# Optimization experiments

Measured on AMD Instinct MI355X. Metric: run time of the kernel, lower is better.

## Reference

```python
import math
import jax, jax.numpy as jnp
import numpy as np

DIM = 512; DEPTH = 12; HEADS = 8; DIM_HEAD = 64
INNER = HEADS * DIM_HEAD
FF_INNER = 4 * DIM
B = 8192
NUM_TIMESTEPS = 1000
SCALE = 16.0  # cosine_sim_scale
ROT_DIM = 32  # RotaryEmbedding(dim=min(32, dim_head))
NUM_BUCKETS = 32; MAX_DISTANCE = 128


def layer_norm(x, g, eps=1e-5):
    mean = jnp.mean(x, axis=-1, keepdims=True)
    var = jnp.mean((x - mean) ** 2, axis=-1, keepdims=True)  # unbiased=False
    return (x - mean) * jax.lax.rsqrt(var + eps) * g


def l2norm(t):
    n = jnp.linalg.norm(t, axis=-1, keepdims=True)
    return t / jnp.maximum(n, 1e-12)


def rotary_freqs(n):
    inv = 1.0 / (10000.0 ** (jnp.arange(0, ROT_DIM, 2, dtype=jnp.float32) / ROT_DIM))
    f = jnp.arange(n, dtype=jnp.float32)[:, None] * inv[None, :]  # (n, ROT_DIM//2)
    return jnp.repeat(f, 2, axis=-1)  # (n, ROT_DIM), interleaved pairs


def rotate_half(x):
    x1 = x[..., 0::2]; x2 = x[..., 1::2]
    return jnp.stack((-x2, x1), axis=-1).reshape(x.shape)


def apply_rotary(t, freqs):
    tr, tp = t[..., :ROT_DIM], t[..., ROT_DIM:]
    tr = tr * jnp.cos(freqs) + rotate_half(tr) * jnp.sin(freqs)
    return jnp.concatenate([tr, tp], axis=-1)


def rel_pos_bias(i, j, emb):
    rel = jnp.arange(j)[None, :] - jnp.arange(i)[:, None]
    n = jnp.maximum(-rel, 0)
    max_exact = NUM_BUCKETS // 2
    nf = jnp.maximum(n, 1).astype(jnp.float32)
    val_large = max_exact + (jnp.log(nf / max_exact) / math.log(MAX_DISTANCE / max_exact) * (NUM_BUCKETS - max_exact)).astype(jnp.int32)
    val_large = jnp.minimum(val_large, NUM_BUCKETS - 1)
    bucket = jnp.where(n < max_exact, n, val_large)
    return emb[bucket].transpose(2, 0, 1)  # (h, i, j)


def setup_inputs() -> dict:
    key = jax.random.key(0)
    ks = jax.random.split(key, 13)
    w = 0.02
    return {
        "image_embed": jax.random.normal(ks[0], (B, DIM), jnp.float32),
        "text_embed": jax.random.normal(ks[1], (B, DIM), jnp.float32),
        "timesteps": jax.random.randint(ks[2], (B,), 0, NUM_TIMESTEPS),
        "time_emb_table": jax.random.normal(ks[3], (NUM_TIMESTEPS, DIM)) * w,
        "learned_query": jax.random.normal(ks[4], (DIM,)),
        "rel_emb": jax.random.normal(ks[5], (NUM_BUCKETS, HEADS)) * w,
        "attn_norm_g": jnp.ones((DEPTH, DIM)),
        "Wq": jax.random.normal(ks[6], (DEPTH, DIM, INNER)) * w,
        "Wkv": jax.random.normal(ks[7], (DEPTH, DIM, 2 * DIM_HEAD)) * w,
        "null_kv": jax.random.normal(ks[8], (DEPTH, 2, DIM_HEAD)),
        "Wo": jax.random.normal(ks[9], (DEPTH, INNER, DIM)) * w,
        "attn_out_norm_g": jnp.ones((DEPTH, DIM)),
        "ff_norm_g": jnp.ones((DEPTH, DIM)),
        "Wff1": jax.random.normal(ks[10], (DEPTH, DIM, 2 * FF_INNER)) * w,
        "Wff2": jax.random.normal(ks[11], (DEPTH, FF_INNER, DIM)) * w,
        "final_norm_g": jnp.ones((DIM,)),
        "Wproj": jax.random.normal(ks[12], (DIM, DIM)) * w,
    }


def reference(image_embed, text_embed, timesteps, time_emb_table, learned_query, rel_emb,
              attn_norm_g, Wq, Wkv, null_kv, Wo, attn_out_norm_g,
              ff_norm_g, Wff1, Wff2, final_norm_g, Wproj):
    b = image_embed.shape[0]
    # token sequence: [text_embed, time_embed, image_embed, learned_query] -> (b, 4, dim)
    tokens = jnp.concatenate([
        text_embed[:, None, :],
        time_emb_table[timesteps][:, None, :],
        image_embed[:, None, :],
        jnp.broadcast_to(learned_query, (b, 1, DIM)),
    ], axis=1)
    n = tokens.shape[1]
    bias = rel_pos_bias(n, n + 1, rel_emb)            # (h, n, n+1)
    freqs = rotary_freqs(n)                           # (n, ROT_DIM)
    causal = jnp.triu(jnp.ones((n, n + 1), dtype=bool), k=2)
    neg = -jnp.finfo(jnp.float32).max
    sqrt_scale = math.sqrt(SCALE)

    x = tokens
    for l in range(DEPTH):
        # --- Attention ---
        h = layer_norm(x, attn_norm_g[l])
        q = (h @ Wq[l]).reshape(b, n, HEADS, DIM_HEAD).transpose(0, 2, 1, 3) * SCALE
        kv = h @ Wkv[l]
        k, v = kv[..., :DIM_HEAD], kv[..., DIM_HEAD:]  # single-head kv (b, n, d)
        q = apply_rotary(q, freqs)
        k = apply_rotary(k, freqs)
        nk = jnp.broadcast_to(null_kv[l, 0], (b, 1, DIM_HEAD))
        nv = jnp.broadcast_to(null_kv[l, 1], (b, 1, DIM_HEAD))
        k = jnp.concatenate([nk, k], axis=1)
        v = jnp.concatenate([nv, v], axis=1)
        q = l2norm(q) * sqrt_scale
        k = l2norm(k) * sqrt_scale
        sim = jnp.einsum('bhid,bjd->bhij', q, k) + bias[None]
        sim = jnp.where(causal[None, None], neg, sim)
        attn = jax.nn.softmax(sim.astype(jnp.float32), axis=-1).astype(sim.dtype)
        out = jnp.einsum('bhij,bjd->bhid', attn, v).transpose(0, 2, 1, 3).reshape(b, n, INNER)
        x = x + layer_norm(out @ Wo[l], attn_out_norm_g[l])
        # --- SwiGLU FFN ---
        h = layer_norm(x, ff_norm_g[l])
        hg = h @ Wff1[l]
        a, g = hg[..., :FF_INNER], hg[..., FF_INNER:]
        x = x + (a * jax.nn.silu(g)) @ Wff2[l]

    x = layer_norm(x, final_norm_g) @ Wproj
    return x[:, -1, :]  # predicted image embed from learned query position
```

## Files before the change

kernel.cpp:

```cpp
#include <hip/hip_runtime.h>

typedef __bf16 bf16x8 __attribute__((ext_vector_type(8)));
typedef __bf16 bf16x4 __attribute__((ext_vector_type(4)));
typedef __bf16 bf16x2 __attribute__((ext_vector_type(2)));
typedef float  f32x4  __attribute__((ext_vector_type(4)));
typedef unsigned short u16;

#define BATCH   8192
#define NTOK    4
#define ROWS    (BATCH*NTOK)
#define DIM     512
#define HEADS   8
#define DH      64
#define FFI     2048
#define DEPTH   12
#define LN_EPS  1e-5f

static const size_t OFF_WQKV = 0;
static const size_t SZ_WQKV  = 12ull*640*512*2;
static const size_t OFF_WTO  = OFF_WQKV + SZ_WQKV;
static const size_t SZ_WTO   = 12ull*512*512*2;
static const size_t OFF_WTF1 = OFF_WTO + SZ_WTO;
static const size_t SZ_WTF1  = 12ull*4096*512*2;
static const size_t OFF_WTF2 = OFF_WTF1 + SZ_WTF1;
static const size_t SZ_WTF2  = 12ull*512*2048*2;
static const size_t OFF_WTP  = OFF_WTF2 + SZ_WTF2;
static const size_t SZ_WTP   = 512ull*512*2;
static const size_t OFF_X    = OFF_WTP + SZ_WTP;
static const size_t OFF_H    = OFF_X    + (size_t)ROWS*DIM*4;
static const size_t OFF_QKV  = OFF_H    + (size_t)ROWS*DIM*2;
static const size_t OFF_AO   = OFF_QKV  + (size_t)ROWS*640*2;
static const size_t OFF_FLAG = OFF_AO   + (size_t)ROWS*DIM*2;
static const size_t WS_NEED  = OFF_FLAG + 256;

__device__ __forceinline__ float ldf(const void* p, size_t i, bool b16) {
  return b16 ? (float)((const __bf16*)p)[i] : ((const float*)p)[i];
}

__device__ __forceinline__ void gld_lds16(const void* g, void* l) {
  __builtin_amdgcn_global_load_lds((const __attribute__((address_space(1))) void*)g,
                                   (__attribute__((address_space(3))) void*)l, 16, 0, 0);
}

__device__ __forceinline__ float gsum16(float v) {
  #pragma unroll
  for (int o = 8; o > 0; o >>= 1) v += __shfl_xor(v, o, 64);
  return v;
}

__device__ __forceinline__ void block_reduce2(float& a, float& b, float* sm) {
  #pragma unroll
  for (int o = 32; o > 0; o >>= 1) { a += __shfl_down(a, o, 64); b += __shfl_down(b, o, 64); }
  int lane = threadIdx.x & 63, w = threadIdx.x >> 6;
  __syncthreads();
  if (lane == 0) { sm[w] = a; sm[4+w] = b; }
  __syncthreads();
  a = sm[0]+sm[1]+sm[2]+sm[3];
  b = sm[4]+sm[5]+sm[6]+sm[7];
}

__global__ void detect_dtype(const unsigned int* __restrict__ w, int* __restrict__ flag) {
  __shared__ int cnt[4];
  int t = threadIdx.x;
  int c = 0;
  for (int i = t; i < 2048; i += 256) {
    unsigned int v = w[i];
    unsigned int lo = v & 0xFFFFu, hi = v >> 16;
    int elo = (int)((lo >> 7) & 0xFF), ehi = (int)((hi >> 7) & 0xFF);
    bool okl = (lo == 0u) || (elo >= 100 && elo <= 140);
    bool okh = (hi == 0u) || (ehi >= 100 && ehi <= 140);
    if (okl && okh) c++;
  }
  #pragma unroll
  for (int o = 32; o > 0; o >>= 1) c += __shfl_down(c, o, 64);
  if ((t & 63) == 0) cnt[t >> 6] = c;
  __syncthreads();
  if (t == 0) flag[0] = (cnt[0] + cnt[1] + cnt[2] + cnt[3] > 1024) ? 1 : 0;
}

__global__ void transpose_any(const void* __restrict__ in, u16* __restrict__ out,
                              int K, int N, size_t out_zsz, int rowoff, int mode,
                              const int* __restrict__ flag) {
  bool b16 = flag[0] != 0;
  __shared__ u16 tile[32][33];
  size_t iboff = (size_t)blockIdx.z * K * N;
  size_t oboff = (size_t)blockIdx.z * out_zsz;
  int n0 = blockIdx.x * 32, k0 = blockIdx.y * 32;
  int tx = threadIdx.x, ty = threadIdx.y;
  #pragma unroll
  for (int r = 0; r < 4; r++) {
    float v = ldf(in, iboff + (size_t)(k0 + ty*4 + r) * N + n0 + tx, b16);
    __bf16 bv = (__bf16)v;
    tile[ty*4+r][tx] = __builtin_bit_cast(u16, bv);
  }
  __syncthreads();
  int rbase;
  if (mode == 0) rbase = rowoff + n0;
  else {
    int s = (n0 >= 2048) ? 1 : 0;
    int np = n0 - s*2048;
    rbase = (np >> 7)*256 + ((np >> 5) & 3)*64 + s*32;
  }
  #pragma unroll
  for (int r = 0; r < 4; r++)
    out[oboff + (size_t)(rbase + ty*4 + r) * K + k0 + tx] = tile[tx][ty*4+r];
}

__global__ void build_tokens(const void* __restrict__ text, const void* __restrict__ img,
                             const int* __restrict__ ts, const void* __restrict__ table,
                             const void* __restrict__ lq, float* __restrict__ x,
                             const int* __restrict__ flag) {
  bool b16 = flag[0] != 0;
  int b = blockIdx.x, t = threadIdx.x;
  float* xr = x + (size_t)b * NTOK * DIM;
  int tsb = ts[b];
  for (int e = t; e < DIM; e += 256) {
    xr[e]         = ldf(text,  (size_t)b * DIM + e, b16);
    xr[DIM + e]   = ldf(table, (size_t)tsb * DIM + e, b16);
    xr[2*DIM + e] = ldf(img,   (size_t)b * DIM + e, b16);
    xr[3*DIM + e] = ldf(lq,    (size_t)e, b16);
  }
}

__global__ void ln_f32_bf16(const float* __restrict__ x, const void* __restrict__ g, size_t goff,
                            __bf16* __restrict__ out, const int* __restrict__ flag) {
  bool b16 = flag[0] != 0;
  __shared__ float sm[8];
  int row = blockIdx.x, t = threadIdx.x;
  float2 v = ((const float2*)(x + (size_t)row * DIM))[t];
  float s = v.x + v.y, s2 = v.x*v.x + v.y*v.y;
  block_reduce2(s, s2, sm);
  float mean = s * (1.f/DIM);
  float var  = s2 * (1.f/DIM) - mean*mean;
  float rs = rsqrtf(var + LN_EPS);
  float g0 = ldf(g, goff + 2*t, b16), g1 = ldf(g, goff + 2*t + 1, b16);
  bf16x2 o2 = { (__bf16)((v.x-mean)*rs*g0), (__bf16)((v.y-mean)*rs*g1) };
  ((bf16x2*)(out + (size_t)row * DIM))[t] = o2;
}

__global__ void ln_add_ln(const __bf16* __restrict__ y,
                          const void* __restrict__ g1, size_t g1off,
                          const void* __restrict__ g2, size_t g2off,
                          float* __restrict__ x, __bf16* __restrict__ h,
                          const int* __restrict__ flag) {
  bool b16 = flag[0] != 0;
  __shared__ float sm[8];
  int row = blockIdx.x, t = threadIdx.x;
  bf16x2 yv = ((const bf16x2*)(y + (size_t)row * DIM))[t];
  float v0 = (float)yv[0], v1 = (float)yv[1];
  float s = v0 + v1, s2 = v0*v0 + v1*v1;
  block_reduce2(s, s2, sm);
  float mean = s * (1.f/DIM);
  float var  = s2 * (1.f/DIM) - mean*mean;
  float rs = rsqrtf(var + LN_EPS);
  float ga = ldf(g1, g1off + 2*t, b16), gb = ldf(g1, g1off + 2*t + 1, b16);
  float2* xr = (float2*)(x + (size_t)row * DIM);
  float2 xv = xr[t];
  xv.x += (v0-mean)*rs*ga;
  xv.y += (v1-mean)*rs*gb;
  xr[t] = xv;
  float s_  = xv.x + xv.y, s2_ = xv.x*xv.x + xv.y*xv.y;
  block_reduce2(s_, s2_, sm);
  float mean2 = s_ * (1.f/DIM);
  float var2  = s2_ * (1.f/DIM) - mean2*mean2;
  float rs2 = rsqrtf(var2 + LN_EPS);
  float gc = ldf(g2, g2off + 2*t, b16), gd = ldf(g2, g2off + 2*t + 1, b16);
  bf16x2 o2 = { (__bf16)((xv.x-mean2)*rs2*gc), (__bf16)((xv.y-mean2)*rs2*gd) };
  ((bf16x2*)(h + (size_t)row * DIM))[t] = o2;
}

__global__ void ln_final(const float* __restrict__ x, const void* __restrict__ g,
                         __bf16* __restrict__ out, const int* __restrict__ flag) {
  bool b16 = flag[0] != 0;
  __shared__ float sm[8];
  int b = blockIdx.x, t = threadIdx.x;
  int row = b*NTOK + 3;
  float2 v = ((const float2*)(x + (size_t)row * DIM))[t];
  float s = v.x + v.y, s2 = v.x*v.x + v.y*v.y;
  block_reduce2(s, s2, sm);
  float mean = s * (1.f/DIM);
  float var  = s2 * (1.f/DIM) - mean*mean;
  float rs = rsqrtf(var + LN_EPS);
  float g0 = ldf(g, (size_t)2*t, b16), g1 = ldf(g, (size_t)2*t + 1, b16);
  bf16x2 o2 = { (__bf16)((v.x-mean)*rs*g0), (__bf16)((v.y-mean)*rs*g1) };
  ((bf16x2*)(out + (size_t)b * DIM))[t] = o2;
}

template<int BROWS, int EPI>
__global__ __launch_bounds__(512, 2) void gemm8(
    const __bf16* __restrict__ A, int lda,
    const __bf16* __restrict__ B, int ldb,
    void* __restrict__ Cv, int ldc, int K, const int* __restrict__ flag)
{
  constexpr int UNITS = (BROWS == 256) ? 4 : 3;
  constexpr int WCN   = (BROWS == 256) ? 4 : 2;
  constexpr int M_FR  = (BROWS == 256) ? 8 : 4;
  constexpr int QM    = M_FR / 4;
  __shared__ char ldsmem[2][(256 + BROWS) * 128];

  const int tid = threadIdx.x;
  const int wid = tid >> 6, lane = tid & 63;
  const int wr = wid / WCN, wc = wid % WCN;
  const int lr = lane & 15, lc = lane >> 4;
  const int sr = tid >> 3;
  const int cs = ((tid & 7) ^ (sr & 7)) * 8;
  const int bx = blockIdx.x, by = blockIdx.y;

  const __bf16* Ab = A + (size_t)by * 256 * lda;
  const __bf16* Bb = B + (size_t)bx * BROWS * ldb;

  f32x4 acc[M_FR][4] = {};
  const int NT = K >> 6;

  char* lds0 = ldsmem[0];
  char* lds1 = ldsmem[1];

  auto stage_unit = [&](int p, int kt, int u) {
    char* base = (p ? lds1 : lds0);
    if (u < 2) {
      const __bf16* s = Ab + (size_t)(u*128 + sr) * lda + kt*64 + cs;
      char* d = base + u*16384 + (wid << 10);
      gld_lds16(s, d);
      gld_lds16(s + (size_t)64 * lda, d + 8192);
    } else {
      const __bf16* s = Bb + (size_t)((u-2)*128 + sr) * ldb + kt*64 + cs;
      char* d = base + 32768 + (u-2)*16384 + (wid << 10);
      gld_lds16(s, d);
      gld_lds16(s + (size_t)64 * ldb, d + 8192);
    }
  };

  #pragma unroll
  for (int u = 0; u < UNITS; u++) stage_unit(0, 0, u);

  const int NIT = NT >> 1;
  for (int i = 0; i < NIT; i++) {
    const int t1 = 2*i + 1;
    const int t2 = (2*i + 2 < NT) ? (2*i + 2) : 0;
    #pragma unroll
    for (int hfl = 0; hfl < 2; hfl++) {
      char* cbase = hfl ? lds1 : lds0;
      const int sp = hfl ^ 1;
      const int st = hfl ? t2 : t1;
      bf16x8 bfr[4][2];
      #pragma unroll
      for (int q = 0; q < 4; q++) {
        if (q < UNITS) stage_unit(sp, st, q);
        if (q == 0) {
          asm volatile("s_waitcnt vmcnt(2)" ::: "memory");
          asm volatile("s_barrier" ::: "memory");
          #pragma unroll
          for (int f = 0; f < 4; f++)
            #pragma unroll
            for (int kk = 0; kk < 2; kk++) {
              int row = wc*64 + f*16 + lr;
              int ch = (kk*4 + lc) ^ (lr & 7);
              bfr[f][kk] = *(const bf16x8*)(cbase + 32768 + row*128 + ch*16);
            }
        }
        bf16x8 afr[QM][2];
        #pragma unroll
        for (int m2 = 0; m2 < QM; m2++)
          #pragma unroll
          for (int kk = 0; kk < 2; kk++) {
            int row = wr*(M_FR*16) + (q*QM + m2)*16 + lr;
            int ch = (kk*4 + lc) ^ (lr & 7);
            afr[m2][kk] = *(const bf16x8*)(cbase + row*128 + ch*16);
          }
        __builtin_amdgcn_s_setprio(1);
        #pragma unroll
        for (int m2 = 0; m2 < QM; m2++)
          #pragma unroll
          for (int n = 0; n < 4; n++)
            #pragma unroll
            for (int kk = 0; kk < 2; kk++)
              acc[q*QM + m2][n] = __builtin_amdgcn_mfma_f32_16x16x32_bf16(
                  afr[m2][kk], bfr[n][kk], acc[q*QM + m2][n], 0, 0, 0);
        __builtin_amdgcn_s_setprio(0);
        asm volatile("s_barrier" ::: "memory");
      }
    }
  }

  if (EPI == 1) {
    __bf16* Ob = (__bf16*)Cv;
    const int colb = bx*128 + wc*32 + lr;
    const int rowb = by*256 + wr*128 + lc*4;
    #pragma unroll
    for (int m = 0; m < M_FR; m++)
      #pragma unroll
      for (int rr = 0; rr < 4; rr++) {
        size_t ro = (size_t)(rowb + m*16 + rr) * ldc;
        #pragma unroll
        for (int fa = 0; fa < 2; fa++) {
          float a = acc[m][fa][rr], g = acc[m][fa+2][rr];
          Ob[ro + colb + fa*16] = (__bf16)(a * g / (1.f + __expf(-g)));
        }
      }
  } else if (EPI == 2) {
    float* Xf = (float*)Cv;
    const int colb = bx*BROWS + wc*64 + lr;
    const int rowb = by*256 + wr*(M_FR*16) + lc*4;
    #pragma unroll
    for (int m = 0; m < M_FR; m++)
      #pragma unroll
      for (int rr = 0; rr < 4; rr++) {
        size_t ro = (size_t)(rowb + m*16 + rr) * ldc;
        #pragma unroll
        for (int n = 0; n < 4; n++) Xf[ro + colb + n*16] += acc[m][n][rr];
      }
  } else if (EPI == 0) {
    __bf16* Cb = (__bf16*)Cv;
    const int colb = bx*BROWS + wc*64 + lr;
    const int rowb = by*256 + wr*(M_FR*16) + lc*4;
    #pragma unroll
    for (int m = 0; m < M_FR; m++)
      #pragma unroll
      for (int rr = 0; rr < 4; rr++) {
        size_t ro = (size_t)(rowb + m*16 + rr) * ldc;
        #pragma unroll
        for (int n = 0; n < 4; n++) Cb[ro + colb + n*16] = (__bf16)acc[m][n][rr];
      }
  } else {
    bool b16o = flag[0] != 0;
    __bf16* Cb = (__bf16*)Cv;
    float*  Cf = (float*)Cv;
    const int colb = bx*BROWS + wc*64 + lr;
    const int rowb = by*256 + wr*(M_FR*16) + lc*4;
    #pragma unroll
    for (int m = 0; m < M_FR; m++)
      #pragma unroll
      for (int rr = 0; rr < 4; rr++) {
        size_t ro = (size_t)(rowb + m*16 + rr) * ldc;
        #pragma unroll
        for (int n = 0; n < 4; n++) {
          float val = acc[m][n][rr];
          if (b16o) Cb[ro + colb + n*16] = (__bf16)val; else Cf[ro + colb + n*16] = val;
        }
      }
  }
}

__global__ __launch_bounds__(256) void attn_kernel(
    const __bf16* __restrict__ qkv,
    const void* __restrict__ nkv_all, int layer, const void* __restrict__ rel_emb,
    __bf16* __restrict__ ao, const int* __restrict__ flag)
{
  bool b16 = flag[0] != 0;
  const int tid = threadIdx.x;
  const int w = tid >> 6, l = tid & 63;
  const int g = l >> 4, c = l & 15;
  const int bh = blockIdx.x * 16 + w * 4 + g;
  const int b = bh >> 3, h = bh & 7;
  const bool rot = (c < 8);

  const float LN1E4_32 = 9.210340371976184f * (1.f/32.f);
  float inv0 = __expf(-(float)(4*c)     * LN1E4_32);
  float inv1 = __expf(-(float)(4*c + 2) * LN1E4_32);
  float cs0[4], sn0[4], cs1[4], sn1[4];
  #pragma unroll
  for (int t = 0; t < 4; t++) {
    __sincosf((float)t * inv0, &sn0[t], &cs0[t]);
    __sincosf((float)t * inv1, &sn1[t], &cs1[t]);
  }
  float rb[4];
  #pragma unroll
  for (int t = 0; t < 4; t++) rb[t] = ldf(rel_emb, (size_t)t * 8 + h, b16);

  float q[4][4];
  #pragma unroll
  for (int i = 0; i < 4; i++) {
    bf16x4 qv = *(const bf16x4*)(qkv + ((size_t)(b*NTOK + i)) * 640 + h*DH + c*4);
    float v0 = (float)qv[0], v1 = (float)qv[1], v2 = (float)qv[2], v3 = (float)qv[3];
    if (rot) {
      float n0 = v0*cs0[i] - v1*sn0[i], n1 = v1*cs0[i] + v0*sn0[i];
      float n2 = v2*cs1[i] - v3*sn1[i], n3 = v3*cs1[i] + v2*sn1[i];
      v0 = n0; v1 = n1; v2 = n2; v3 = n3;
    }
    q[i][0] = v0; q[i][1] = v1; q[i][2] = v2; q[i][3] = v3;
  }
  #pragma unroll
  for (int i = 0; i < 4; i++) {
    float ss = q[i][0]*q[i][0] + q[i][1]*q[i][1] + q[i][2]*q[i][2] + q[i][3]*q[i][3];
    float r = 1.f / fmaxf(sqrtf(gsum16(ss)), 1e-12f);
    #pragma unroll
    for (int e = 0; e < 4; e++) q[i][e] *= r;
  }

  float kk[5][4], vv[5][4];
  #pragma unroll
  for (int e = 0; e < 4; e++) {
    kk[0][e] = ldf(nkv_all, (size_t)layer*128 + c*4 + e, b16);
    vv[0][e] = ldf(nkv_all, (size_t)layer*128 + 64 + c*4 + e, b16);
  }
  #pragma unroll
  for (int j = 1; j < 5; j++) {
    const __bf16* base = qkv + ((size_t)(b*NTOK + j - 1)) * 640 + 512;
    bf16x4 kv4 = *(const bf16x4*)(base + c*4);
    bf16x4 vv4 = *(const bf16x4*)(base + 64 + c*4);
    float v0 = (float)kv4[0], v1 = (float)kv4[1], v2 = (float)kv4[2], v3 = (float)kv4[3];
    if (rot) {
      int t = j - 1;
      float n0 = v0*cs0[t] - v1*sn0[t], n1 = v1*cs0[t] + v0*sn0[t];
      float n2 = v2*cs1[t] - v3*sn1[t], n3 = v3*cs1[t] + v2*sn1[t];
      v0 = n0; v1 = n1; v2 = n2; v3 = n3;
    }
    kk[j][0] = v0; kk[j][1] = v1; kk[j][2] = v2; kk[j][3] = v3;
    #pragma unroll
    for (int e = 0; e < 4; e++) vv[j][e] = (float)vv4[e];
  }
  #pragma unroll
  for (int j = 0; j < 5; j++) {
    float ss = kk[j][0]*kk[j][0] + kk[j][1]*kk[j][1] + kk[j][2]*kk[j][2] + kk[j][3]*kk[j][3];
    float r = 1.f / fmaxf(sqrtf(gsum16(ss)), 1e-12f);
    #pragma unroll
    for (int e = 0; e < 4; e++) kk[j][e] *= r;
  }

  #pragma unroll
  for (int i = 0; i < 4; i++) {
    float sim[5];
    #pragma unroll
    for (int j = 0; j < 5; j++) {
      if (j > i + 1) break;
      float pp = q[i][0]*kk[j][0] + q[i][1]*kk[j][1] + q[i][2]*kk[j][2] + q[i][3]*kk[j][3];
      sim[j] = 16.f * gsum16(pp) + rb[(i - j > 0) ? (i - j) : 0];
    }
    float m = sim[0];
    #pragma unroll
    for (int j = 1; j < 5; j++) { if (j > i + 1) break; m = fmaxf(m, sim[j]); }
    float Z = 0.f, o0 = 0.f, o1 = 0.f, o2 = 0.f, o3 = 0.f;
    #pragma unroll
    for (int j = 0; j < 5; j++) {
      if (j > i + 1) break;
      float e = __expf(sim[j] - m);
      Z += e;
      o0 += e * vv[j][0]; o1 += e * vv[j][1]; o2 += e * vv[j][2]; o3 += e * vv[j][3];
    }
    float rz = 1.f / Z;
    bf16x4 ov = { (__bf16)(o0*rz), (__bf16)(o1*rz), (__bf16)(o2*rz), (__bf16)(o3*rz) };
    *(bf16x4*)(ao + ((size_t)(b*NTOK + i)) * DIM + h*DH + c*4) = ov;
  }
}

extern "C" void kernel_launch(void* const* d_in, const int* in_sizes, int n_in,
                              void* d_out, int out_size, void* d_ws, size_t ws_size,
                              hipStream_t stream) {
  const void* image_embed     = d_in[0];
  const void* text_embed      = d_in[1];
  const int*  timesteps       = (const int*)d_in[2];
  const void* time_table      = d_in[3];
  const void* learned_query   = d_in[4];
  const void* rel_emb         = d_in[5];
  const void* attn_norm_g     = d_in[6];
  const void* Wq              = d_in[7];
  const void* Wkv             = d_in[8];
  const void* null_kv         = d_in[9];
  const void* Wo              = d_in[10];
  const void* attn_out_norm_g = d_in[11];
  const void* ff_norm_g       = d_in[12];
  const void* Wff1            = d_in[13];
  const void* Wff2            = d_in[14];
  const void* final_norm_g    = d_in[15];
  const void* Wproj           = d_in[16];

  if (ws_size < WS_NEED) return;

  char* ws = (char*)d_ws;
  __bf16* wqkv = (__bf16*)(ws + OFF_WQKV);
  __bf16* wto  = (__bf16*)(ws + OFF_WTO);
  __bf16* wtf1 = (__bf16*)(ws + OFF_WTF1);
  __bf16* wtf2 = (__bf16*)(ws + OFF_WTF2);
  __bf16* wtp  = (__bf16*)(ws + OFF_WTP);
  float*  x    = (float*) (ws + OFF_X);
  __bf16* h    = (__bf16*)(ws + OFF_H);
  __bf16* qkv  = (__bf16*)(ws + OFF_QKV);
  __bf16* ao   = (__bf16*)(ws + OFF_AO);
  __bf16* act  = (__bf16*)(ws + OFF_QKV);
  int*    flag = (int*)   (ws + OFF_FLAG);

  detect_dtype<<<1, 256, 0, stream>>>((const unsigned int*)Wq, flag);

  dim3 tb(32, 8);
  transpose_any<<<dim3(16, 16, 12),  tb, 0, stream>>>(Wq,   (u16*)wqkv, 512,  512,  640ull*512, 0,   0, flag);
  transpose_any<<<dim3(4,  16, 12),  tb, 0, stream>>>(Wkv,  (u16*)wqkv, 512,  128,  640ull*512, 512, 0, flag);
  transpose_any<<<dim3(16, 16, 12),  tb, 0, stream>>>(Wo,   (u16*)wto,  512,  512,  512ull*512, 0,   0, flag);
  transpose_any<<<dim3(128,16, 12),  tb, 0, stream>>>(Wff1, (u16*)wtf1, 512,  4096, 4096ull*512,0,   1, flag);
  transpose_any<<<dim3(16, 64, 12),  tb, 0, stream>>>(Wff2, (u16*)wtf2, 2048, 512,  512ull*2048,0,   0, flag);
  transpose_any<<<dim3(16, 16, 1),   tb, 0, stream>>>(Wproj,(u16*)wtp,  512,  512,  512ull*512, 0,   0, flag);

  build_tokens<<<BATCH, 256, 0, stream>>>(text_embed, image_embed, timesteps, time_table,
                                          learned_query, x, flag);

  for (int l = 0; l < DEPTH; l++) {
    const __bf16* wqkv_l = wqkv + (size_t)l * 640 * 512;
    const __bf16* wto_l  = wto  + (size_t)l * 512 * 512;
    const __bf16* wtf1_l = wtf1 + (size_t)l * 4096 * 512;
    const __bf16* wtf2_l = wtf2 + (size_t)l * 512 * 2048;

    ln_f32_bf16<<<ROWS, 256, 0, stream>>>(x, attn_norm_g, (size_t)l*DIM, h, flag);
    gemm8<128,0><<<dim3(5, 128), 512, 0, stream>>>(h, DIM, wqkv_l, 512, qkv, 640, 512, flag);
    attn_kernel<<<BATCH/2, 256, 0, stream>>>(qkv, null_kv, l, rel_emb, ao, flag);
    gemm8<128,0><<<dim3(4, 128), 512, 0, stream>>>(ao, DIM, wto_l, 512, qkv , DIM, 512, flag);
    ln_add_ln<<<ROWS, 256, 0, stream>>>(qkv , attn_out_norm_g, (size_t)l*DIM,
                                        ff_norm_g, (size_t)l*DIM, x, h, flag);

    for (int c = 0; c < 2; c++) {
      const __bf16* hc = h + (size_t)c * 16384 * DIM;
      float*        xc = x + (size_t)c * 16384 * DIM;
      gemm8<256,1><<<dim3(16, 64), 512, 0, stream>>>(hc, DIM, wtf1_l, 512, act, FFI, 512, flag);
      gemm8<128,2><<<dim3(4, 64), 512, 0, stream>>>(act, FFI, wtf2_l, FFI, xc, DIM, 2048, flag);
    }
  }

  ln_final<<<BATCH, 256, 0, stream>>>(x, final_norm_g, ao , flag);
  gemm8<128,3><<<dim3(4, 32), 512, 0, stream>>>(ao, DIM, wtp, 512, d_out, DIM, 512, flag);
}
```

Baseline: 5.390 ms.

## Use one wavefront per row for layernorms and simplify GEMM K-loop pipeline

The layernorm kernels now assign one 64-lane wavefront per row with 8 elements per lane. Reductions use only wave shuffles, with vectorized float4 and bf16x8 loads and stores in place of block-level LDS reductions and two barriers, so the grid shrinks by 4x. The GEMM main loop is rewritten from an interleaved staged-per-quarter pipeline to a simpler per-k-tile double buffer: it issues all loads for the next tile up front, then waits and computes. This may lose the finer-grained overlap of loads with MFMA work that the old schedule had.

After: 5.809 ms. +7.8%, slower.

```diff
diff --git a/kernel.cpp b/kernel.cpp
--- a/kernel.cpp
+++ b/kernel.cpp
@@ -48,15 +48,9 @@
   return v;
 }
 
-__device__ __forceinline__ void block_reduce2(float& a, float& b, float* sm) {
-  #pragma unroll
-  for (int o = 32; o > 0; o >>= 1) { a += __shfl_down(a, o, 64); b += __shfl_down(b, o, 64); }
-  int lane = threadIdx.x & 63, w = threadIdx.x >> 6;
-  __syncthreads();
-  if (lane == 0) { sm[w] = a; sm[4+w] = b; }
-  __syncthreads();
-  a = sm[0]+sm[1]+sm[2]+sm[3];
-  b = sm[4]+sm[5]+sm[6]+sm[7];
+__device__ __forceinline__ void wred2(float& a, float& b) {
+  #pragma unroll
+  for (int o = 32; o > 0; o >>= 1) { a += __shfl_xor(a, o, 64); b += __shfl_xor(b, o, 64); }
 }
 
 __global__ void detect_dtype(const unsigned int* __restrict__ w, int* __restrict__ flag) {
@@ -125,17 +119,23 @@
 __global__ void ln_f32_bf16(const float* __restrict__ x, const void* __restrict__ g, size_t goff,
                             __bf16* __restrict__ out, const int* __restrict__ flag) {
   bool b16 = flag[0] != 0;
-  __shared__ float sm[8];
-  int row = blockIdx.x, t = threadIdx.x;
-  float2 v = ((const float2*)(x + (size_t)row * DIM))[t];
-  float s = v.x + v.y, s2 = v.x*v.x + v.y*v.y;
-  block_reduce2(s, s2, sm);
+  int lane = threadIdx.x & 63;
+  int row = blockIdx.x * 4 + (threadIdx.x >> 6);
+  const float4* xr = (const float4*)(x + (size_t)row * DIM);
+  float4 A4 = xr[lane*2], B4 = xr[lane*2 + 1];
+  float v[8] = {A4.x, A4.y, A4.z, A4.w, B4.x, B4.y, B4.z, B4.w};
+  float s = 0.f, s2 = 0.f;
+  #pragma unroll
+  for (int e = 0; e < 8; e++) { s += v[e]; s2 += v[e]*v[e]; }
+  wred2(s, s2);
   float mean = s * (1.f/DIM);
   float var  = s2 * (1.f/DIM) - mean*mean;
   float rs = rsqrtf(var + LN_EPS);
-  float g0 = ldf(g, goff + 2*t, b16), g1 = ldf(g, goff + 2*t + 1, b16);
-  bf16x2 o2 = { (__bf16)((v.x-mean)*rs*g0), (__bf16)((v.y-mean)*rs*g1) };
-  ((bf16x2*)(out + (size_t)row * DIM))[t] = o2;
+  bf16x8 ov;
+  #pragma unroll
+  for (int e = 0; e < 8; e++)
+    ov[e] = (__bf16)((v[e]-mean) * rs * ldf(g, goff + lane*8 + e, b16));
+  *(bf16x8*)(out + (size_t)row * DIM + lane*8) = ov;
 }
 
 __global__ void ln_add_ln(const __bf16* __restrict__ y,
@@ -144,46 +144,60 @@
                           float* __restrict__ x, __bf16* __restrict__ h,
                           const int* __restrict__ flag) {
   bool b16 = flag[0] != 0;
-  __shared__ float sm[8];
-  int row = blockIdx.x, t = threadIdx.x;
-  bf16x2 yv = ((const bf16x2*)(y + (size_t)row * DIM))[t];
-  float v0 = (float)yv[0], v1 = (float)yv[1];
-  float s = v0 + v1, s2 = v0*v0 + v1*v1;
-  block_reduce2(s, s2, sm);
+  int lane = threadIdx.x & 63;
+  int row = blockIdx.x * 4 + (threadIdx.x >> 6);
+  bf16x8 y8 = *(const bf16x8*)(y + (size_t)row * DIM + lane*8);
+  float yv[8];
+  float s = 0.f, s2 = 0.f;
+  #pragma unroll
+  for (int e = 0; e < 8; e++) { yv[e] = (float)y8[e]; s += yv[e]; s2 += yv[e]*yv[e]; }
+  wred2(s, s2);
   float mean = s * (1.f/DIM);
   float var  = s2 * (1.f/DIM) - mean*mean;
   float rs = rsqrtf(var + LN_EPS);
-  float ga = ldf(g1, g1off + 2*t, b16), gb = ldf(g1, g1off + 2*t + 1, b16);
-  float2* xr = (float2*)(x + (size_t)row * DIM);
-  float2 xv = xr[t];
-  xv.x += (v0-mean)*rs*ga;
-  xv.y += (v1-mean)*rs*gb;
-  xr[t] = xv;
-  float s_  = xv.x + xv.y, s2_ = xv.x*xv.x + xv.y*xv.y;
-  block_reduce2(s_, s2_, sm);
-  float mean2 = s_ * (1.f/DIM);
-  float var2  = s2_ * (1.f/DIM) - mean2*mean2;
+  float4* xr = (float4*)(x + (size_t)row * DIM);
+  float4 XA = xr[lane*2], XB = xr[lane*2 + 1];
+  float xv[8] = {XA.x, XA.y, XA.z, XA.w, XB.x, XB.y, XB.z, XB.w};
+  #pragma unroll
+  for (int e = 0; e < 8; e++)
+    xv[e] += (yv[e]-mean) * rs * ldf(g1, g1off + lane*8 + e, b16);
+  xr[lane*2]     = make_float4(xv[0], xv[1], xv[2], xv[3]);
+  xr[lane*2 + 1] = make_float4(xv[4], xv[5], xv[6], xv[7]);
+  float t = 0.f, t2 = 0.f;
+  #pragma unroll
+  for (int e = 0; e < 8; e++) { t += xv[e]; t2 += xv[e]*xv[e]; }
+  wred2(t, t2);
+  float mean2 = t * (1.f/DIM);
+  float var2  = t2 * (1.f/DIM) - mean2*mean2;
   float rs2 = rsqrtf(var2 + LN_EPS);
-  float gc = ldf(g2, g2off + 2*t, b16), gd = ldf(g2, g2off + 2*t + 1, b16);
-  bf16x2 o2 = { (__bf16)((xv.x-mean2)*rs2*gc), (__bf16)((xv.y-mean2)*rs2*gd) };
-  ((bf16x2*)(h + (size_t)row * DIM))[t] = o2;
+  bf16x8 hv;
+  #pragma unroll
+  for (int e = 0; e < 8; e++)
+    hv[e] = (__bf16)((xv[e]-mean2) * rs2 * ldf(g2, g2off + lane*8 + e, b16));
+  *(bf16x8*)(h + (size_t)row * DIM + lane*8) = hv;
 }
 
 __global__ void ln_final(const float* __restrict__ x, const void* __restrict__ g,
                          __bf16* __restrict__ out, const int* __restrict__ flag) {
   bool b16 = flag[0] != 0;
-  __shared__ float sm[8];
-  int b = blockIdx.x, t = threadIdx.x;
+  int lane = threadIdx.x & 63;
+  int b = blockIdx.x * 4 + (threadIdx.x >> 6);
   int row = b*NTOK + 3;
-  float2 v = ((const float2*)(x + (size_t)row * DIM))[t];
-  float s = v.x + v.y, s2 = v.x*v.x + v.y*v.y;
-  block_reduce2(s, s2, sm);
+  const float4* xr = (const float4*)(x + (size_t)row * DIM);
+  float4 A4 = xr[lane*2], B4 = xr[lane*2 + 1];
+  float v[8] = {A4.x, A4.y, A4.z, A4.w, B4.x, B4.y, B4.z, B4.w};
+  float s = 0.f, s2 = 0.f;
+  #pragma unroll
+  for (int e = 0; e < 8; e++) { s += v[e]; s2 += v[e]*v[e]; }
+  wred2(s, s2);
   float mean = s * (1.f/DIM);
   float var  = s2 * (1.f/DIM) - mean*mean;
   float rs = rsqrtf(var + LN_EPS);
-  float g0 = ldf(g, (size_t)2*t, b16), g1 = ldf(g, (size_t)2*t + 1, b16);
-  bf16x2 o2 = { (__bf16)((v.x-mean)*rs*g0), (__bf16)((v.y-mean)*rs*g1) };
-  ((bf16x2*)(out + (size_t)b * DIM))[t] = o2;
+  bf16x8 ov;
+  #pragma unroll
+  for (int e = 0; e < 8; e++)
+    ov[e] = (__bf16)((v[e]-mean) * rs * ldf(g, (size_t)lane*8 + e, b16));
+  *(bf16x8*)(out + (size_t)b * DIM + lane*8) = ov;
 }
 
 template<int BROWS, int EPI>
@@ -195,7 +209,6 @@
   constexpr int UNITS = (BROWS == 256) ? 4 : 3;
   constexpr int WCN   = (BROWS == 256) ? 4 : 2;
   constexpr int M_FR  = (BROWS == 256) ? 8 : 4;
-  constexpr int QM    = M_FR / 4;
   __shared__ char ldsmem[2][(256 + BROWS) * 128];
 
   const int tid = threadIdx.x;
@@ -215,8 +228,7 @@
   char* lds0 = ldsmem[0];
   char* lds1 = ldsmem[1];
 
-  auto stage_unit = [&](int p, int kt, int u) {
-    char* base = (p ? lds1 : lds0);
+  auto stage_unit = [&](char* base, int kt, int u) {
     if (u < 2) {
       const __bf16* s = Ab + (size_t)(u*128 + sr) * lda + kt*64 + cs;
       char* d = base + u*16384 + (wid << 10);
@@ -231,56 +243,46 @@
   };
 
   #pragma unroll
-  for (int u = 0; u < UNITS; u++) stage_unit(0, 0, u);
-
-  const int NIT = NT >> 1;
-  for (int i = 0; i < NIT; i++) {
-    const int t1 = 2*i + 1;
-    const int t2 = (2*i + 2 < NT) ? (2*i + 2) : 0;
-    #pragma unroll
-    for (int hfl = 0; hfl < 2; hfl++) {
-      char* cbase = hfl ? lds1 : lds0;
-      const int sp = hfl ^ 1;
-      const int st = hfl ? t2 : t1;
-      bf16x8 bfr[4][2];
-      #pragma unroll
-      for (int q = 0; q < 4; q++) {
-        if (q < UNITS) stage_unit(sp, st, q);
-        if (q == 0) {
-          asm volatile("s_waitcnt vmcnt(2)" ::: "memory");
-          asm volatile("s_barrier" ::: "memory");
-          #pragma unroll
-          for (int f = 0; f < 4; f++)
-            #pragma unroll
-            for (int kk = 0; kk < 2; kk++) {
-              int row = wc*64 + f*16 + lr;
-              int ch = (kk*4 + lc) ^ (lr & 7);
-              bfr[f][kk] = *(const bf16x8*)(cbase + 32768 + row*128 + ch*16);
-            }
-        }
-        bf16x8 afr[QM][2];
+  for (int u = 0; u < UNITS; u++) stage_unit(lds0, 0, u);
+
+  for (int t = 0; t < NT; t++) {
+    char* cbase = (t & 1) ? lds1 : lds0;
+    char* sbase = (t & 1) ? lds0 : lds1;
+    const int st = (t + 1 < NT) ? (t + 1) : 0;
+    #pragma unroll
+    for (int u = 0; u < UNITS; u++) stage_unit(sbase, st, u);
+    asm volatile("s_waitcnt vmcnt(%0)" :: "i"(2*UNITS) : "memory");
+    asm volatile("s_barrier" ::: "memory");
+    bf16x8 bfr[4][2];
+    #pragma unroll
+    for (int f = 0; f < 4; f++)
+      #pragma unroll
+      for (int kk = 0; kk < 2; kk++) {
+        int row = wc*64 + f*16 + lr;
+        int ch = (kk*4 + lc) ^ (lr & 7);
+        bfr[f][kk] = *(const bf16x8*)(cbase + 32768 + row*128 + ch*16);
+      }
+    __builtin_amdgcn_s_setprio(1);
+    #pragma unroll
+    for (int m = 0; m < M_FR; m++) {
+      bf16x8 afr[2];
+      #pragma unroll
+      for (int kk = 0; kk < 2; kk++) {
+        int row = wr*(M_FR*16) + m*16 + lr;
+        int ch = (kk*4 + lc) ^ (lr & 7);
+        afr[kk] = *(const bf16x8*)(cbase + row*128 + ch*16);
+      }
+      #pragma unroll
+      for (int n = 0; n < 4; n++)
         #pragma unroll
-        for (int m2 = 0; m2 < QM; m2++)
-          #pragma unroll
-          for (int kk = 0; kk < 2; kk++) {
-            int row = wr*(M_FR*16) + (q*QM + m2)*16 + lr;
-            int ch = (kk*4 + lc) ^ (lr & 7);
-            afr[m2][kk] = *(const bf16x8*)(cbase + row*128 + ch*16);
-          }
-        __builtin_amdgcn_s_setprio(1);
-        #pragma unroll
-        for (int m2 = 0; m2 < QM; m2++)
-          #pragma unroll
-          for (int n = 0; n < 4; n++)
-            #pragma unroll
-            for (int kk = 0; kk < 2; kk++)
-              acc[q*QM + m2][n] = __builtin_amdgcn_mfma_f32_16x16x32_bf16(
-                  afr[m2][kk], bfr[n][kk], acc[q*QM + m2][n], 0, 0, 0);
-        __builtin_amdgcn_s_setprio(0);
-        asm volatile("s_barrier" ::: "memory");
-      }
-    }
-  }
+        for (int kk = 0; kk < 2; kk++)
+          acc[m][n] = __builtin_amdgcn_mfma_f32_16x16x32_bf16(
+              afr[kk], bfr[n][kk], acc[m][n], 0, 0, 0);
+    }
+    __builtin_amdgcn_s_setprio(0);
+    asm volatile("s_barrier" ::: "memory");
+  }
+  asm volatile("s_waitcnt vmcnt(0)" ::: "memory");
 
   if (EPI == 1) {
     __bf16* Ob = (__bf16*)Cv;
@@ -498,12 +500,12 @@
     const __bf16* wtf1_l = wtf1 + (size_t)l * 4096 * 512;
     const __bf16* wtf2_l = wtf2 + (size_t)l * 512 * 2048;
 
-    ln_f32_bf16<<<ROWS, 256, 0, stream>>>(x, attn_norm_g, (size_t)l*DIM, h, flag);
+    ln_f32_bf16<<<ROWS/4, 256, 0, stream>>>(x, attn_norm_g, (size_t)l*DIM, h, flag);
     gemm8<128,0><<<dim3(5, 128), 512, 0, stream>>>(h, DIM, wqkv_l, 512, qkv, 640, 512, flag);
     attn_kernel<<<BATCH/2, 256, 0, stream>>>(qkv, null_kv, l, rel_emb, ao, flag);
     gemm8<128,0><<<dim3(4, 128), 512, 0, stream>>>(ao, DIM, wto_l, 512, qkv , DIM, 512, flag);
-    ln_add_ln<<<ROWS, 256, 0, stream>>>(qkv , attn_out_norm_g, (size_t)l*DIM,
-                                        ff_norm_g, (size_t)l*DIM, x, h, flag);
+    ln_add_ln<<<ROWS/4, 256, 0, stream>>>(qkv , attn_out_norm_g, (size_t)l*DIM,
+                                          ff_norm_g, (size_t)l*DIM, x, h, flag);
 
     for (int c = 0; c < 2; c++) {
       const __bf16* hc = h + (size_t)c * 16384 * DIM;
@@ -513,6 +515,6 @@
     }
   }
 
-  ln_final<<<BATCH, 256, 0, stream>>>(x, final_norm_g, ao , flag);
+  ln_final<<<BATCH/4, 256, 0, stream>>>(x, final_norm_g, ao , flag);
   gemm8<128,3><<<dim3(4, 32), 512, 0, stream>>>(ao, DIM, wtp, 512, d_out, DIM, 512, flag);
 }
```

## Compute only the last token's query path in the final transformer layer

Applied to the files above, without the earlier changes.

Because only the learned-query position is output, the last layer now computes K/V for all tokens but Q, attention output, out-projection, FFN and final norm only for the last token per batch. New kernels gather the last-token rows, run single-query attention with rotary at position 3, and fuse the residual LayerNorms on the reduced rows. This cuts roughly three quarters of the last layer's GEMM and elementwise work, at the cost of extra kernel launches and a gather step. The skipped work is provably not needed for the output, so this is a legitimate dead-code elimination.

Measured after the change: 5.142 ms. 1.05x faster.

```diff
diff --git a/kernel.cpp b/kernel.cpp
--- a/kernel.cpp
+++ b/kernel.cpp
@@ -169,13 +169,42 @@
   ((bf16x2*)(h + (size_t)row * DIM))[t] = o2;
 }
 
-__global__ void ln_final(const float* __restrict__ x, const void* __restrict__ g,
-                         __bf16* __restrict__ out, const int* __restrict__ flag) {
+__global__ void ln_add3(const __bf16* __restrict__ y3,
+                        const void* __restrict__ g1, size_t g1off,
+                        const void* __restrict__ g2, size_t g2off,
+                        const float* __restrict__ xfull, float* __restrict__ x3,
+                        __bf16* __restrict__ h3b, const int* __restrict__ flag) {
+  bool b16 = flag[0] != 0;
+  __shared__ float sm[8];
+  int r = blockIdx.x, t = threadIdx.x;
+  bf16x2 yv = ((const bf16x2*)(y3 + (size_t)r * DIM))[t];
+  float v0 = (float)yv[0], v1 = (float)yv[1];
+  float s = v0 + v1, s2 = v0*v0 + v1*v1;
+  block_reduce2(s, s2, sm);
+  float mean = s * (1.f/DIM);
+  float var  = s2 * (1.f/DIM) - mean*mean;
+  float rs = rsqrtf(var + LN_EPS);
+  float ga = ldf(g1, g1off + 2*t, b16), gb = ldf(g1, g1off + 2*t + 1, b16);
+  float2 xv = ((const float2*)(xfull + (size_t)(r*NTOK + 3) * DIM))[t];
+  xv.x += (v0-mean)*rs*ga;
+  xv.y += (v1-mean)*rs*gb;
+  ((float2*)(x3 + (size_t)r * DIM))[t] = xv;
+  float s_  = xv.x + xv.y, s2_ = xv.x*xv.x + xv.y*xv.y;
+  block_reduce2(s_, s2_, sm);
+  float mean2 = s_ * (1.f/DIM);
+  float var2  = s2_ * (1.f/DIM) - mean2*mean2;
+  float rs2 = rsqrtf(var2 + LN_EPS);
+  float gc = ldf(g2, g2off + 2*t, b16), gd = ldf(g2, g2off + 2*t + 1, b16);
+  bf16x2 o2 = { (__bf16)((xv.x-mean2)*rs2*gc), (__bf16)((xv.y-mean2)*rs2*gd) };
+  ((bf16x2*)(h3b + (size_t)r * DIM))[t] = o2;
+}
+
+__global__ void ln_final3(const float* __restrict__ x3, const void* __restrict__ g,
+                          __bf16* __restrict__ out, const int* __restrict__ flag) {
   bool b16 = flag[0] != 0;
   __shared__ float sm[8];
   int b = blockIdx.x, t = threadIdx.x;
-  int row = b*NTOK + 3;
-  float2 v = ((const float2*)(x + (size_t)row * DIM))[t];
+  float2 v = ((const float2*)(x3 + (size_t)b * DIM))[t];
   float s = v.x + v.y, s2 = v.x*v.x + v.y*v.y;
   block_reduce2(s, s2, sm);
   float mean = s * (1.f/DIM);
@@ -184,6 +213,13 @@
   float g0 = ldf(g, (size_t)2*t, b16), g1 = ldf(g, (size_t)2*t + 1, b16);
   bf16x2 o2 = { (__bf16)((v.x-mean)*rs*g0), (__bf16)((v.y-mean)*rs*g1) };
   ((bf16x2*)(out + (size_t)b * DIM))[t] = o2;
+}
+
+__global__ void gather3(const __bf16* __restrict__ h, __bf16* __restrict__ h3) {
+  int lane = threadIdx.x & 63;
+  int r = blockIdx.x * 4 + (threadIdx.x >> 6);
+  *(bf16x8*)(h3 + (size_t)r * DIM + lane*8) =
+      *(const bf16x8*)(h + (size_t)(r*NTOK + 3) * DIM + lane*8);
 }
 
 template<int BROWS, int EPI>
@@ -443,6 +479,97 @@
   }
 }
 
+__global__ __launch_bounds__(256) void attn_kernel3(
+    const __bf16* __restrict__ q3, const __bf16* __restrict__ qkv,
+    const void* __restrict__ nkv_all, int layer, const void* __restrict__ rel_emb,
+    __bf16* __restrict__ ao3, const int* __restrict__ flag)
+{
+  bool b16 = flag[0] != 0;
+  const int tid = threadIdx.x;
+  const int w = tid >> 6, l = tid & 63;
+  const int g = l >> 4, c = l & 15;
+  const int bh = blockIdx.x * 16 + w * 4 + g;
+  const int b = bh >> 3, h = bh & 7;
+  const bool rot = (c < 8);
+
+  const float LN1E4_32 = 9.210340371976184f * (1.f/32.f);
+  float inv0 = __expf(-(float)(4*c)     * LN1E4_32);
+  float inv1 = __expf(-(float)(4*c + 2) * LN1E4_32);
+  float cs0[4], sn0[4], cs1[4], sn1[4];
+  #pragma unroll
+  for (int t = 0; t < 4; t++) {
+    __sincosf((float)t * inv0, &sn0[t], &cs0[t]);
+    __sincosf((float)t * inv1, &sn1[t], &cs1[t]);
+  }
+  float rb[4];
+  #pragma unroll
+  for (int t = 0; t < 4; t++) rb[t] = ldf(rel_emb, (size_t)t * 8 + h, b16);
+
+  float q[4];
+  {
+    bf16x4 qv = *(const bf16x4*)(q3 + (size_t)b * DIM + h*DH + c*4);
+    float v0 = (float)qv[0], v1 = (float)qv[1], v2 = (float)qv[2], v3 = (float)qv[3];
+    if (rot) {
+      float n0 = v0*cs0[3] - v1*sn0[3], n1 = v1*cs0[3] + v0*sn0[3];
+      float n2 = v2*cs1[3] - v3*sn1[3], n3 = v3*cs1[3] + v2*sn1[3];
+      v0 = n0; v1 = n1; v2 = n2; v3 = n3;
+    }
+    float ss = v0*v0 + v1*v1 + v2*v2 + v3*v3;
+    float r = 1.f / fmaxf(sqrtf(gsum16(ss)), 1e-12f);
+    q[0] = v0*r; q[1] = v1*r; q[2] = v2*r; q[3] = v3*r;
+  }
+
+  float kk[5][4], vv[5][4];
+  #pragma unroll
+  for (int e = 0; e < 4; e++) {
+    kk[0][e] = ldf(nkv_all, (size_t)layer*128 + c*4 + e, b16);
+    vv[0][e] = ldf(nkv_all, (size_t)layer*128 + 64 + c*4 + e, b16);
+  }
+  #pragma unroll
+  for (int j = 1; j < 5; j++) {
+    const __bf16* base = qkv + ((size_t)(b*NTOK + j - 1)) * 640 + 512;
+    bf16x4 kv4 = *(const bf16x4*)(base + c*4);
+    bf16x4 vv4 = *(const bf16x4*)(base + 64 + c*4);
+    float v0 = (float)kv4[0], v1 = (float)kv4[1], v2 = (float)kv4[2], v3 = (float)kv4[3];
+    if (rot) {
+      int t = j - 1;
+      float n0 = v0*cs0[t] - v1*sn0[t], n1 = v1*cs0[t] + v0*sn0[t];
+      float n2 = v2*cs1[t] - v3*sn1[t], n3 = v3*cs1[t] + v2*sn1[t];
+      v0 = n0; v1 = n1; v2 = n2; v3 = n3;
+    }
+    kk[j][0] = v0; kk[j][1] = v1; kk[j][2] = v2; kk[j][3] = v3;
+    #pragma unroll
+    for (int e = 0; e < 4; e++) vv[j][e] = (float)vv4[e];
+  }
+  #pragma unroll
+  for (int j = 0; j < 5; j++) {
+    float ss = kk[j][0]*kk[j][0] + kk[j][1]*kk[j][1] + kk[j][2]*kk[j][2] + kk[j][3]*kk[j][3];
+    float r = 1.f / fmaxf(sqrtf(gsum16(ss)), 1e-12f);
+    #pragma unroll
+    for (int e = 0; e < 4; e++) kk[j][e] *= r;
+  }
+
+  float sim[5];
+  #pragma unroll
+  for (int j = 0; j < 5; j++) {
+    float pp = q[0]*kk[j][0] + q[1]*kk[j][1] + q[2]*kk[j][2] + q[3]*kk[j][3];
+    sim[j] = 16.f * gsum16(pp) + rb[(3 - j > 0) ? (3 - j) : 0];
+  }
+  float m = sim[0];
+  #pragma unroll
+  for (int j = 1; j < 5; j++) m = fmaxf(m, sim[j]);
+  float Z = 0.f, o0 = 0.f, o1 = 0.f, o2 = 0.f, o3 = 0.f;
+  #pragma unroll
+  for (int j = 0; j < 5; j++) {
+    float e = __expf(sim[j] - m);
+    Z += e;
+    o0 += e * vv[j][0]; o1 += e * vv[j][1]; o2 += e * vv[j][2]; o3 += e * vv[j][3];
+  }
+  float rz = 1.f / Z;
+  bf16x4 ov = { (__bf16)(o0*rz), (__bf16)(o1*rz), (__bf16)(o2*rz), (__bf16)(o3*rz) };
+  *(bf16x4*)(ao3 + (size_t)b * DIM + h*DH + c*4) = ov;
+}
+
 extern "C" void kernel_launch(void* const* d_in, const int* in_sizes, int n_in,
                               void* d_out, int out_size, void* d_ws, size_t ws_size,
                               hipStream_t stream) {
@@ -478,6 +605,12 @@
   __bf16* ao   = (__bf16*)(ws + OFF_AO);
   __bf16* act  = (__bf16*)(ws + OFF_QKV);
   int*    flag = (int*)   (ws + OFF_FLAG);
+  __bf16* h3    = (__bf16*)(ws + OFF_AO);
+  __bf16* q3    = (__bf16*)(ws + OFF_AO + 8388608);
+  __bf16* ao3   = (__bf16*)(ws + OFF_AO + 16777216);
+  __bf16* y3    = (__bf16*)(ws + OFF_AO + 25165824);
+  float*  x3    = (float*) (ws + OFF_H);
+  __bf16* act3  = (__bf16*)(ws + OFF_QKV);
 
   detect_dtype<<<1, 256, 0, stream>>>((const unsigned int*)Wq, flag);
 
@@ -492,7 +625,7 @@
   build_tokens<<<BATCH, 256, 0, stream>>>(text_embed, image_embed, timesteps, time_table,
                                           learned_query, x, flag);
 
-  for (int l = 0; l < DEPTH; l++) {
+  for (int l = 0; l < DEPTH - 1; l++) {
     const __bf16* wqkv_l = wqkv + (size_t)l * 640 * 512;
     const __bf16* wto_l  = wto  + (size_t)l * 512 * 512;
     const __bf16* wtf1_l = wtf1 + (size_t)l * 4096 * 512;
@@ -513,6 +646,25 @@
     }
   }
 
-  ln_final<<<BATCH, 256, 0, stream>>>(x, final_norm_g, ao , flag);
-  gemm8<128,3><<<dim3(4, 32), 512, 0, stream>>>(ao, DIM, wtp, 512, d_out, DIM, 512, flag);
-}
+  {
+    const int l = DEPTH - 1;
+    const __bf16* wq_l   = wqkv + (size_t)l * 640 * 512;
+    const __bf16* wkv_l  = wq_l + (size_t)512 * 512;
+    const __bf16* wto_l  = wto  + (size_t)l * 512 * 512;
+    const __bf16* wtf1_l = wtf1 + (size_t)l * 4096 * 512;
+    const __bf16* wtf2_l = wtf2 + (size_t)l * 512 * 2048;
+
+    ln_f32_bf16<<<ROWS, 256, 0, stream>>>(x, attn_norm_g, (size_t)l*DIM, h, flag);
+    gather3<<<BATCH/4, 256, 0, stream>>>(h, h3);
+    gemm8<128,0><<<dim3(1, 128), 512, 0, stream>>>(h, DIM, wkv_l, 512, qkv + 512, 640, 512, flag);
+    gemm8<128,0><<<dim3(4, 32),  512, 0, stream>>>(h3, DIM, wq_l, 512, q3, DIM, 512, flag);
+    attn_kernel3<<<BATCH*HEADS/16, 256, 0, stream>>>(q3, qkv, null_kv, l, rel_emb, ao3, flag);
+    gemm8<128,0><<<dim3(4, 32), 512, 0, stream>>>(ao3, DIM, wto_l, 512, y3, DIM, 512, flag);
+    ln_add3<<<BATCH, 256, 0, stream>>>(y3, attn_out_norm_g, (size_t)l*DIM,
+                                       ff_norm_g, (size_t)l*DIM, x, x3, h3 , flag);
+    gemm8<256,1><<<dim3(16, 32), 512, 0, stream>>>(h3 , DIM, wtf1_l, 512, act3, FFI, 512, flag);
+    gemm8<128,2><<<dim3(4, 32), 512, 0, stream>>>(act3, FFI, wtf2_l, FFI, x3, DIM, 2048, flag);
+    ln_final3<<<BATCH, 256, 0, stream>>>(x3, final_norm_g, q3 , flag);
+    gemm8<128,3><<<dim3(4, 32), 512, 0, stream>>>(q3 , DIM, wtp, 512, d_out, DIM, 512, flag);
+  }
+}
```
